# Kernel optimization log

Measured on AMD Instinct MI355X. Metric: run time of the kernel, lower is better.

## Reference

```python
import jax, jax.numpy as jnp
import numpy as np

K = 5
P = 1.5
MU = 0.01
N_NODES = 100000
N_EDGES = 1600000
D_FEAT = 32


def setup_inputs() -> dict:
    key = jax.random.key(0)
    k1, k2 = jax.random.split(key)
    h = jax.random.normal(k1, (N_NODES, D_FEAT), dtype=jnp.float32)
    edge_index = jax.random.randint(k2, (2, N_EDGES), 0, N_NODES, dtype=jnp.int64)
    return {"h": h, "edge_index": edge_index}


def reference(h, edge_index):
    row, col = edge_index[0], edge_index[1]
    for _ in range(K):
        diff = h[row] - h[col]                      # [E, d] gather
        norm_diff = jnp.maximum(jnp.linalg.norm(diff, axis=1), 1e-6)  # [E]
        weights = (norm_diff / norm_diff.max()) ** (P - 2.0)          # [E]
        # agg[r] += sum over edges with row==r of weights * (h[col] - h[row])
        msgs = weights[:, None] * (-diff)           # [E, d]
        agg = jax.ops.segment_sum(msgs, row, num_segments=N_NODES)    # [N, d]
        h = h - MU * agg
    return h
```

## Files before the change

kernel.cpp:

```cpp
#include <hip/hip_runtime.h>

#define NN 100000
#define NE 1600000
#define DF 32
#define KIT 5
#define MU 0.01f
#define NSLOT 256
#define NV4 (NN * DF / 4)
#define ELLW 36
#define AUXCAP 65536
#define NSLICE 8
#define SLICEN (NN / NSLICE)
#define NSUB 20
#define NBLKA (NE / 256)
#define SEGW 64
#define INVALID_PK 0xffffffffu

typedef float f32x4 __attribute__((ext_vector_type(4)));
typedef float f32x2 __attribute__((ext_vector_type(2)));


__global__ __launch_bounds__(64) void zero_kernel(int* __restrict__ p, int n) {
    int i = blockIdx.x * blockDim.x + threadIdx.x;
    if (i < n) p[i] = 0;
}

__global__ __launch_bounds__(256) void ell_part_kernel(const int* __restrict__ row,
                                                       const int* __restrict__ col,
                                                       unsigned int* __restrict__ buck,
                                                       int* __restrict__ auxcnt,
                                                       int2* __restrict__ aux) {
    __shared__ int wcnt[4][8];
    __shared__ int woff[4][8];
    __shared__ unsigned int sseg[8][SEGW];
    const int t = threadIdx.x;
    const int w = t >> 6;
    const int lane = t & 63;

    ((unsigned int*)sseg)[t] = INVALID_PK;
    ((unsigned int*)sseg)[t + 256] = INVALID_PK;

    const int e = blockIdx.x * 256 + t;
    int b = 8;
    unsigned int packed = INVALID_PK;
    int r = 0, c = 0;
    if (e < NE) {
        r = __builtin_nontemporal_load(&row[e]);
        c = __builtin_nontemporal_load(&col[e]);
        b = r / SLICEN;
        const int rl = r - b * SLICEN;
        packed = ((unsigned int)rl << 17) | (unsigned int)c;
    }

    int myprefix = 0;
    #pragma unroll
    for (int k = 0; k < 8; ++k) {
        const unsigned long long mk = __ballot(b == k);
        if (lane == 0) wcnt[w][k] = __popcll(mk);
        if (k == b) myprefix = __popcll(mk & ((1ull << lane) - 1ull));
    }
    __syncthreads();
    if (t < 32) {
        const int w2 = t >> 3, k = t & 7;
        int o = 0;
        for (int w3 = 0; w3 < w2; ++w3) o += wcnt[w3][k];
        woff[w2][k] = o;
    }
    __syncthreads();

    if (b < 8) {
        const int pos = woff[w][b] + myprefix;
        if (pos < SEGW) {
            sseg[b][pos] = packed;
        } else {
            const int a = atomicAdd(auxcnt, 1);
            if (a < AUXCAP) aux[a] = make_int2(r, c);
        }
    }
    __syncthreads();

    #pragma unroll
    for (int k = 0; k < 2; ++k) {
        const int idx = t + k * 256;
        const int bb = idx >> 6;
        const int j = idx & 63;
        buck[((size_t)bb * NBLKA + blockIdx.x) * SEGW + j] = sseg[bb][j];
    }
}

__global__ __launch_bounds__(1024) void ell_count_kernel(const unsigned int* __restrict__ buck,
                                                         unsigned short* __restrict__ cnt) {
    __shared__ int hist[SLICEN];
    const int t = threadIdx.x;
    const int s = blockIdx.x & (NSLICE - 1);
    const int j = blockIdx.x >> 3;
    const int lane = t & 63;
    const int wid = t >> 6;
    const int blo = j * NBLKA / NSUB;
    const int bhi = (j + 1) * NBLKA / NSUB;

    for (int i = t; i < SLICEN; i += 1024) hist[i] = 0;
    __syncthreads();

    const unsigned int* sp = buck + (size_t)s * NBLKA * SEGW;
    int blk = blo + wid;
    unsigned int pk = (blk < bhi) ? sp[(size_t)blk * SEGW + lane] : INVALID_PK;
    for (; blk < bhi; blk += 16) {
        const int nb = blk + 16;
        const unsigned int nx = (nb < bhi) ? sp[(size_t)nb * SEGW + lane] : INVALID_PK;
        const int rl = (int)(pk >> 17);
        if (rl < SLICEN) atomicAdd(&hist[rl], 1);
        pk = nx;
    }
    __syncthreads();
    unsigned short* cp = cnt + ((size_t)s * NSUB + j) * SLICEN;
    for (int i = t; i < SLICEN; i += 1024) cp[i] = (unsigned short)hist[i];
}

__global__ __launch_bounds__(256) void ell_prefix_kernel(unsigned short* __restrict__ cnt,
                                                         int* __restrict__ degc) {
    const int i = blockIdx.x * blockDim.x + threadIdx.x;
    if (i >= NN) return;
    const int s = i / SLICEN;
    const int rl = i - s * SLICEN;
    unsigned short* cp = cnt + (size_t)s * NSUB * SLICEN + rl;
    int base = 0;
    #pragma unroll
    for (int j = 0; j < NSUB; ++j) {
        const int v = cp[(size_t)j * SLICEN];
        cp[(size_t)j * SLICEN] = (unsigned short)base;
        base += v;
    }
    degc[i] = base;
}

__global__ __launch_bounds__(1024) void ell_place_kernel(const unsigned int* __restrict__ buck,
                                                         const unsigned short* __restrict__ cnt,
                                                         int* __restrict__ colell,
                                                         int* __restrict__ auxcnt,
                                                         int2* __restrict__ aux) {
    __shared__ int cur[SLICEN];
    const int t = threadIdx.x;
    const int s = blockIdx.x & (NSLICE - 1);
    const int j = blockIdx.x >> 3;
    const int lane = t & 63;
    const int wid = t >> 6;
    const int blo = j * NBLKA / NSUB;
    const int bhi = (j + 1) * NBLKA / NSUB;

    const unsigned short* cp = cnt + ((size_t)s * NSUB + j) * SLICEN;
    for (int i = t; i < SLICEN; i += 1024) cur[i] = (int)cp[i];
    __syncthreads();

    const unsigned int* sp = buck + (size_t)s * NBLKA * SEGW;
    int blk = blo + wid;
    unsigned int pk = (blk < bhi) ? sp[(size_t)blk * SEGW + lane] : INVALID_PK;
    for (; blk < bhi; blk += 16) {
        const int nb = blk + 16;
        const unsigned int nx = (nb < bhi) ? sp[(size_t)nb * SEGW + lane] : INVALID_PK;
        const int rl = (int)(pk >> 17);
        if (rl < SLICEN) {
            const int c = (int)(pk & 0x1ffffu);
            const int pos = atomicAdd(&cur[rl], 1);
            const int r = s * SLICEN + rl;
            if (pos < ELLW) {
                colell[r * ELLW + pos] = c;
            } else {
                const int a = atomicAdd(auxcnt, 1);
                if (a < AUXCAP) aux[a] = make_int2(r, c);
            }
        }
        pk = nx;
    }
}


__device__ __forceinline__ unsigned int pack2bf(float a, float b) {
    unsigned int ua = __float_as_uint(a);
    unsigned int ub = __float_as_uint(b);
    return ((ua + 0x8000u) >> 16) | (((ub + 0x8000u) >> 16) << 16);
}

__device__ __forceinline__ f32x2 bf2(unsigned int v) {
    f32x2 r;
    r.x = __uint_as_float(v << 16);
    r.y = __uint_as_float(v & 0xffff0000u);
    return r;
}

__global__ __launch_bounds__(256) void tobf16_kernel(const float* __restrict__ h,
                                                     uint2* __restrict__ hb) {
    int i = blockIdx.x * blockDim.x + threadIdx.x;
    if (i < NV4) {
        const f32x4 v = __builtin_nontemporal_load(((const f32x4*)h) + i);
        hb[i] = make_uint2(pack2bf(v.x, v.y), pack2bf(v.z, v.w));
    }
}


__device__ __forceinline__ void node_head(const uint4* __restrict__ u,
                                          const f32x2* __restrict__ hr2,
                                          f32x2* __restrict__ acc, float& nmax) {
    #pragma unroll
    for (int j = 0; j < 4; ++j) {
        f32x2 d0 = hr2[0] - bf2(u[j].x);
        f32x2 d1 = hr2[1] - bf2(u[j].y);
        f32x2 d2 = hr2[2] - bf2(u[j].z);
        f32x2 d3 = hr2[3] - bf2(u[j].w);
        f32x2 s2 = d0 * d0;
        s2 += d1 * d1;
        s2 += d2 * d2;
        s2 += d3 * d3;
        float s = s2.x + s2.y;
        s += __shfl_xor(s, 1, 32);
        s += __shfl_xor(s, 2, 32);
        const float n = fmaxf(sqrtf(s), 1e-6f);
        nmax = fmaxf(nmax, n);
        const float w = -rsqrtf(n);
        acc[0] += d0 * w;
        acc[1] += d1 * w;
        acc[2] += d2 * w;
        acc[3] += d3 * w;
    }
}

__device__ __forceinline__ void node_tail(const uint4* __restrict__ hb4,
                                          const int* __restrict__ colell, int n,
                                          int deg, int q, int f2,
                                          const f32x2* __restrict__ hr2,
                                          f32x2* __restrict__ acc, float& nmax) {
    for (int k = 32; k < deg; k += 8) {
        const int ei = k + q;
        const int c = (ei < deg) ? colell[n * ELLW + ei] : n;
        const uint4 uu = hb4[c * 4 + f2];
        f32x2 d0 = hr2[0] - bf2(uu.x);
        f32x2 d1 = hr2[1] - bf2(uu.y);
        f32x2 d2 = hr2[2] - bf2(uu.z);
        f32x2 d3 = hr2[3] - bf2(uu.w);
        f32x2 s2 = d0 * d0;
        s2 += d1 * d1;
        s2 += d2 * d2;
        s2 += d3 * d3;
        float s = s2.x + s2.y;
        s += __shfl_xor(s, 1, 32);
        s += __shfl_xor(s, 2, 32);
        const float n2 = fmaxf(sqrtf(s), 1e-6f);
        nmax = fmaxf(nmax, n2);
        const float w = -rsqrtf(n2);
        acc[0] += d0 * w;
        acc[1] += d1 * w;
        acc[2] += d2 * w;
        acc[3] += d3 * w;
    }
}

__global__ __launch_bounds__(256) void agg_kernel(const uint4* __restrict__ hb4,
                                                  const int* __restrict__ degc,
                                                  const int* __restrict__ colell,
                                                  float* __restrict__ S,
                                                  int* __restrict__ maxslots) {
    const int lane = threadIdx.x & 31;
    const int q = lane >> 2;
    const int f2 = lane & 3;
    const int pair = (blockIdx.x * blockDim.x + threadIdx.x) >> 5;
    const int n0 = pair * 2;
    const int n1 = n0 + 1;

    const int d0 = min(degc[n0], ELLW);
    const int d1 = min(degc[n1], ELLW);

    const int ca = (lane < d0) ? colell[n0 * ELLW + lane] : n0;
    const int cb = (lane < d1) ? colell[n1 * ELLW + lane] : n1;
    const uint4 hru0 = hb4[n0 * 4 + f2];
    const uint4 hru1 = hb4[n1 * 4 + f2];

    uint4 u0[4], u1[4];
    #pragma unroll
    for (int j = 0; j < 4; ++j) u0[j] = hb4[__shfl(ca, 8 * j + q, 32) * 4 + f2];
    #pragma unroll
    for (int j = 0; j < 4; ++j) u1[j] = hb4[__shfl(cb, 8 * j + q, 32) * 4 + f2];

    f32x2 hr0[4], hr1[4];
    hr0[0] = bf2(hru0.x); hr0[1] = bf2(hru0.y); hr0[2] = bf2(hru0.z); hr0[3] = bf2(hru0.w);
    hr1[0] = bf2(hru1.x); hr1[1] = bf2(hru1.y); hr1[2] = bf2(hru1.z); hr1[3] = bf2(hru1.w);

    f32x2 acc0[4], acc1[4];
    #pragma unroll
    for (int i = 0; i < 4; ++i) {
        acc0[i] = (f32x2){0.0f, 0.0f};
        acc1[i] = (f32x2){0.0f, 0.0f};
    }
    float nmax = 0.0f;

    node_head(u0, hr0, acc0, nmax);
    node_head(u1, hr1, acc1, nmax);

    node_tail(hb4, colell, n0, d0, q, f2, hr0, acc0, nmax);
    node_tail(hb4, colell, n1, d1, q, f2, hr1, acc1, nmax);

    #pragma unroll
    for (int m = 4; m < 32; m <<= 1) {
        #pragma unroll
        for (int i = 0; i < 4; ++i) {
            acc0[i].x += __shfl_xor(acc0[i].x, m, 32);
            acc0[i].y += __shfl_xor(acc0[i].y, m, 32);
            acc1[i].x += __shfl_xor(acc1[i].x, m, 32);
            acc1[i].y += __shfl_xor(acc1[i].y, m, 32);
        }
    }
    if (q == 0) {
        ((float4*)S)[n0 * 8 + f2 * 2] = make_float4(acc0[0].x, acc0[0].y, acc0[1].x, acc0[1].y);
        ((float4*)S)[n0 * 8 + f2 * 2 + 1] = make_float4(acc0[2].x, acc0[2].y, acc0[3].x, acc0[3].y);
        ((float4*)S)[n1 * 8 + f2 * 2] = make_float4(acc1[0].x, acc1[0].y, acc1[1].x, acc1[1].y);
        ((float4*)S)[n1 * 8 + f2 * 2 + 1] = make_float4(acc1[2].x, acc1[2].y, acc1[3].x, acc1[3].y);
    }

    nmax = fmaxf(nmax, __shfl_xor(nmax, 4, 32));
    nmax = fmaxf(nmax, __shfl_xor(nmax, 8, 32));
    nmax = fmaxf(nmax, __shfl_xor(nmax, 16, 32));
    nmax = fmaxf(nmax, __shfl_xor(nmax, 32, 64));
    if ((threadIdx.x & 63) == 0) {
        atomicMax(&maxslots[blockIdx.x & (NSLOT - 1)], __float_as_int(nmax));
    }
}

__global__ __launch_bounds__(256) void aux_kernel(const uint2* __restrict__ hb,
                                                  const int2* __restrict__ aux,
                                                  const int* __restrict__ auxcnt,
                                                  float* __restrict__ S,
                                                  int* __restrict__ maxslots) {
    const int n = min(*auxcnt, AUXCAP);
    for (int i = blockIdx.x * blockDim.x + threadIdx.x; i < n;
         i += gridDim.x * blockDim.x) {
        const int r = aux[i].x;
        const int c = aux[i].y;
        float d[32];
        float s = 0.0f;
        for (int j = 0; j < 8; ++j) {
            const uint2 ur = hb[r * 8 + j];
            const uint2 uc = hb[c * 8 + j];
            float fr[4], fc[4];
            fr[0] = __uint_as_float(ur.x << 16);
            fr[1] = __uint_as_float(ur.x & 0xffff0000u);
            fr[2] = __uint_as_float(ur.y << 16);
            fr[3] = __uint_as_float(ur.y & 0xffff0000u);
            fc[0] = __uint_as_float(uc.x << 16);
            fc[1] = __uint_as_float(uc.x & 0xffff0000u);
            fc[2] = __uint_as_float(uc.y << 16);
            fc[3] = __uint_as_float(uc.y & 0xffff0000u);
            #pragma unroll
            for (int k = 0; k < 4; ++k) {
                d[j * 4 + k] = fr[k] - fc[k];
                s = fmaf(d[j * 4 + k], d[j * 4 + k], s);
            }
        }
        const float nn = fmaxf(sqrtf(s), 1e-6f);
        atomicMax(&maxslots[i & (NSLOT - 1)], __float_as_int(nn));
        const float w = rsqrtf(nn);
        for (int f = 0; f < 32; ++f) atomicAdd(&S[r * DF + f], -d[f] * w);
    }
}

__global__ __launch_bounds__(256) void update_kernel(const float4* __restrict__ hcur,
                                                     float4* __restrict__ hnxt,
                                                     uint2* __restrict__ hb,
                                                     const float4* __restrict__ S,
                                                     const int* __restrict__ slots) {
    const int t = threadIdx.x;
    int v = slots[t];
    #pragma unroll
    for (int m = 32; m > 0; m >>= 1) v = max(v, __shfl_xor(v, m, 64));
    __shared__ int sm[4];
    __shared__ float sscale;
    if ((t & 63) == 0) sm[t >> 6] = v;
    __syncthreads();
    if (t == 0) {
        int bm = max(max(sm[0], sm[1]), max(sm[2], sm[3]));
        sscale = MU * sqrtf(__int_as_float(bm));
    }
    __syncthreads();
    const float scale = sscale;
    const int i = blockIdx.x * blockDim.x + t;
    if (i < NV4) {
        const float4 hv = hcur[i];
        const float4 sv = S[i];
        float4 o;
        o.x = hv.x - scale * sv.x;
        o.y = hv.y - scale * sv.y;
        o.z = hv.z - scale * sv.z;
        o.w = hv.w - scale * sv.w;
        hnxt[i] = o;
        hb[i] = make_uint2(pack2bf(o.x, o.y), pack2bf(o.z, o.w));
    }
}

extern "C" void kernel_launch(void* const* d_in, const int* in_sizes, int n_in,
                              void* d_out, int out_size, void* d_ws, size_t ws_size,
                              hipStream_t stream) {
    const float* h_in = (const float*)d_in[0];
    const int* row = (const int*)d_in[1];
    const int* col = row + NE;
    float* out = (float*)d_out;

    float* S = (float*)d_ws;
    int* maxslots = (int*)(S + NN * DF);
    int* degc = maxslots + KIT * NSLOT;
    int* auxcnt = degc + NN;
    uintptr_t pa = (uintptr_t)(auxcnt + 1);
    pa = (pa + 7) & ~(uintptr_t)7;
    int2* aux = (int2*)pa;
    int* colell = (int*)(aux + AUXCAP);
    uintptr_t p = (uintptr_t)(colell + NN * ELLW);
    p = (p + 15) & ~(uintptr_t)15;
    uint2* hb = (uint2*)p;
    unsigned int* buck = (unsigned int*)S;
    unsigned short* cnt = (unsigned short*)hb;

    const int fb = NSLICE * NSUB;
    const int pb = (NN + 255) / 256;
    const int gb = (NN / 2 * 32 + 255) / 256;
    const int ub = (NV4 + 255) / 256;

    zero_kernel<<<1, 64, 0, stream>>>(auxcnt, 1);
    ell_part_kernel<<<NBLKA, 256, 0, stream>>>(row, col, buck, auxcnt, aux);
    ell_count_kernel<<<fb, 1024, 0, stream>>>(buck, cnt);
    ell_prefix_kernel<<<pb, 256, 0, stream>>>(cnt, degc);
    ell_place_kernel<<<fb, 1024, 0, stream>>>(buck, cnt, colell, auxcnt, aux);
    tobf16_kernel<<<ub, 256, 0, stream>>>(h_in, hb);

    for (int it = 0; it < KIT; ++it) {
        const float* cur = (it == 0) ? h_in : out;
        agg_kernel<<<gb, 256, 0, stream>>>((const uint4*)hb, degc, colell, S,
                                           maxslots + it * NSLOT);
        aux_kernel<<<32, 256, 0, stream>>>(hb, aux, auxcnt, S, maxslots + it * NSLOT);
        update_kernel<<<ub, 256, 0, stream>>>((const float4*)cur, (float4*)out, hb,
                                              (const float4*)S,
                                              maxslots + it * NSLOT);
    }
}
```

Measured before the change: 383.3 us.

## Split neighbor lists by column half and aggregate in two cache-friendly passes

Adds a preprocessing kernel that reorders each node's ELL neighbor list so columns in the lower half of the node range come first, and stores the split count packed into degc. The aggregation then runs twice per iteration, first over low-half neighbors and then over high-half neighbors, accumulating into S. The aim is to keep each pass's gather working set (half of the bf16 feature table) resident in cache. The cost is a second launch, extra reads and writes of S, and less work per subtile for low-degree nodes.

New measurement: 588.0 us. +53.4%, slower.

```diff
diff --git a/kernel.cpp b/kernel.cpp
--- a/kernel.cpp
+++ b/kernel.cpp
@@ -15,6 +15,7 @@
 #define NBLKA (NE / 256)
 #define SEGW 64
 #define INVALID_PK 0xffffffffu
+#define HALF (NN / 2)
 
 typedef float f32x4 __attribute__((ext_vector_type(4)));
 typedef float f32x2 __attribute__((ext_vector_type(2)));
@@ -174,6 +175,26 @@
     }
 }
 
+__global__ __launch_bounds__(256) void ell_split_kernel(int* __restrict__ colell,
+                                                        int* __restrict__ degc) {
+    const int n = (blockIdx.x * blockDim.x + threadIdx.x) >> 6;
+    if (n >= NN) return;
+    const int l = threadIdx.x & 63;
+    const int m = min(degc[n], ELLW);
+    const int c = (l < m) ? colell[n * ELLW + l] : 0;
+    const bool valid = l < m;
+    const unsigned long long lomask = __ballot(valid && (c < HALF));
+    const unsigned long long himask = __ballot(valid && (c >= HALF));
+    const int nlo = __popcll(lomask);
+    const unsigned long long below = (1ull << l) - 1ull;
+    if (valid) {
+        const int pos = (c < HALF) ? __popcll(lomask & below)
+                                   : nlo + __popcll(himask & below);
+        colell[n * ELLW + pos] = c;
+    }
+    if (l == 0) degc[n] = m | (nlo << 8);
+}
+
 
 __device__ __forceinline__ unsigned int pack2bf(float a, float b) {
     unsigned int ua = __float_as_uint(a);
@@ -198,67 +219,34 @@
 }
 
 
-__device__ __forceinline__ void node_head(const uint4* __restrict__ u,
-                                          const f32x2* __restrict__ hr2,
-                                          f32x2* __restrict__ acc, float& nmax) {
-    #pragma unroll
-    for (int j = 0; j < 4; ++j) {
-        f32x2 d0 = hr2[0] - bf2(u[j].x);
-        f32x2 d1 = hr2[1] - bf2(u[j].y);
-        f32x2 d2 = hr2[2] - bf2(u[j].z);
-        f32x2 d3 = hr2[3] - bf2(u[j].w);
-        f32x2 s2 = d0 * d0;
-        s2 += d1 * d1;
-        s2 += d2 * d2;
-        s2 += d3 * d3;
-        float s = s2.x + s2.y;
-        s += __shfl_xor(s, 1, 32);
-        s += __shfl_xor(s, 2, 32);
-        const float n = fmaxf(sqrtf(s), 1e-6f);
-        nmax = fmaxf(nmax, n);
-        const float w = -rsqrtf(n);
-        acc[0] += d0 * w;
-        acc[1] += d1 * w;
-        acc[2] += d2 * w;
-        acc[3] += d3 * w;
-    }
-}
-
-__device__ __forceinline__ void node_tail(const uint4* __restrict__ hb4,
-                                          const int* __restrict__ colell, int n,
-                                          int deg, int q, int f2,
-                                          const f32x2* __restrict__ hr2,
-                                          f32x2* __restrict__ acc, float& nmax) {
-    for (int k = 32; k < deg; k += 8) {
-        const int ei = k + q;
-        const int c = (ei < deg) ? colell[n * ELLW + ei] : n;
-        const uint4 uu = hb4[c * 4 + f2];
-        f32x2 d0 = hr2[0] - bf2(uu.x);
-        f32x2 d1 = hr2[1] - bf2(uu.y);
-        f32x2 d2 = hr2[2] - bf2(uu.z);
-        f32x2 d3 = hr2[3] - bf2(uu.w);
-        f32x2 s2 = d0 * d0;
-        s2 += d1 * d1;
-        s2 += d2 * d2;
-        s2 += d3 * d3;
-        float s = s2.x + s2.y;
-        s += __shfl_xor(s, 1, 32);
-        s += __shfl_xor(s, 2, 32);
-        const float n2 = fmaxf(sqrtf(s), 1e-6f);
-        nmax = fmaxf(nmax, n2);
-        const float w = -rsqrtf(n2);
-        acc[0] += d0 * w;
-        acc[1] += d1 * w;
-        acc[2] += d2 * w;
-        acc[3] += d3 * w;
-    }
+__device__ __forceinline__ void subtile(uint4 uu, const f32x2* __restrict__ hr2,
+                                        f32x2* __restrict__ acc, float& nmax) {
+    f32x2 d0 = hr2[0] - bf2(uu.x);
+    f32x2 d1 = hr2[1] - bf2(uu.y);
+    f32x2 d2 = hr2[2] - bf2(uu.z);
+    f32x2 d3 = hr2[3] - bf2(uu.w);
+    f32x2 s2 = d0 * d0;
+    s2 += d1 * d1;
+    s2 += d2 * d2;
+    s2 += d3 * d3;
+    float s = s2.x + s2.y;
+    s += __shfl_xor(s, 1, 32);
+    s += __shfl_xor(s, 2, 32);
+    const float n = fmaxf(sqrtf(s), 1e-6f);
+    nmax = fmaxf(nmax, n);
+    const float w = -rsqrtf(n);
+    acc[0] += d0 * w;
+    acc[1] += d1 * w;
+    acc[2] += d2 * w;
+    acc[3] += d3 * w;
 }
 
 __global__ __launch_bounds__(256) void agg_kernel(const uint4* __restrict__ hb4,
                                                   const int* __restrict__ degc,
                                                   const int* __restrict__ colell,
                                                   float* __restrict__ S,
-                                                  int* __restrict__ maxslots) {
+                                                  int* __restrict__ maxslots,
+                                                  int phase) {
     const int lane = threadIdx.x & 31;
     const int q = lane >> 2;
     const int f2 = lane & 3;
@@ -266,19 +254,33 @@
     const int n0 = pair * 2;
     const int n1 = n0 + 1;
 
-    const int d0 = min(degc[n0], ELLW);
-    const int d1 = min(degc[n1], ELLW);
-
-    const int ca = (lane < d0) ? colell[n0 * ELLW + lane] : n0;
-    const int cb = (lane < d1) ? colell[n1 * ELLW + lane] : n1;
+    const int v0 = degc[n0];
+    const int v1 = degc[n1];
+    const int m0 = v0 & 0xff, nlo0 = v0 >> 8;
+    const int m1 = v1 & 0xff, nlo1 = v1 >> 8;
+    const int b0 = phase ? nlo0 : 0;
+    const int e0 = phase ? m0 : nlo0;
+    const int b1 = phase ? nlo1 : 0;
+    const int e1 = phase ? m1 : nlo1;
+    const int t0 = (e0 - b0 + 7) >> 3;
+    const int t1 = (e1 - b1 + 7) >> 3;
+
     const uint4 hru0 = hb4[n0 * 4 + f2];
     const uint4 hru1 = hb4[n1 * 4 + f2];
 
-    uint4 u0[4], u1[4];
-    #pragma unroll
-    for (int j = 0; j < 4; ++j) u0[j] = hb4[__shfl(ca, 8 * j + q, 32) * 4 + f2];
-    #pragma unroll
-    for (int j = 0; j < 4; ++j) u1[j] = hb4[__shfl(cb, 8 * j + q, 32) * 4 + f2];
+    int c0[2], c1[2];
+    #pragma unroll
+    for (int j = 0; j < 2; ++j) {
+        const int s0 = b0 + 8 * j + q;
+        c0[j] = (s0 < e0) ? __builtin_nontemporal_load(&colell[n0 * ELLW + s0]) : n0;
+        const int s1 = b1 + 8 * j + q;
+        c1[j] = (s1 < e1) ? __builtin_nontemporal_load(&colell[n1 * ELLW + s1]) : n1;
+    }
+    uint4 u0[2], u1[2];
+    if (0 < t0) u0[0] = hb4[c0[0] * 4 + f2];
+    if (0 < t1) u1[0] = hb4[c1[0] * 4 + f2];
+    if (1 < t0) u0[1] = hb4[c0[1] * 4 + f2];
+    if (1 < t1) u1[1] = hb4[c1[1] * 4 + f2];
 
     f32x2 hr0[4], hr1[4];
     hr0[0] = bf2(hru0.x); hr0[1] = bf2(hru0.y); hr0[2] = bf2(hru0.z); hr0[3] = bf2(hru0.w);
@@ -292,11 +294,21 @@
     }
     float nmax = 0.0f;
 
-    node_head(u0, hr0, acc0, nmax);
-    node_head(u1, hr1, acc1, nmax);
-
-    node_tail(hb4, colell, n0, d0, q, f2, hr0, acc0, nmax);
-    node_tail(hb4, colell, n1, d1, q, f2, hr1, acc1, nmax);
+    if (0 < t0) subtile(u0[0], hr0, acc0, nmax);
+    if (0 < t1) subtile(u1[0], hr1, acc1, nmax);
+    if (1 < t0) subtile(u0[1], hr0, acc0, nmax);
+    if (1 < t1) subtile(u1[1], hr1, acc1, nmax);
+
+    for (int j = 2; j < t0; ++j) {
+        const int s0 = b0 + 8 * j + q;
+        const int c = (s0 < e0) ? __builtin_nontemporal_load(&colell[n0 * ELLW + s0]) : n0;
+        subtile(hb4[c * 4 + f2], hr0, acc0, nmax);
+    }
+    for (int j = 2; j < t1; ++j) {
+        const int s1 = b1 + 8 * j + q;
+        const int c = (s1 < e1) ? __builtin_nontemporal_load(&colell[n1 * ELLW + s1]) : n1;
+        subtile(hb4[c * 4 + f2], hr1, acc1, nmax);
+    }
 
     #pragma unroll
     for (int m = 4; m < 32; m <<= 1) {
@@ -309,10 +321,21 @@
         }
     }
     if (q == 0) {
-        ((float4*)S)[n0 * 8 + f2 * 2] = make_float4(acc0[0].x, acc0[0].y, acc0[1].x, acc0[1].y);
-        ((float4*)S)[n0 * 8 + f2 * 2 + 1] = make_float4(acc0[2].x, acc0[2].y, acc0[3].x, acc0[3].y);
-        ((float4*)S)[n1 * 8 + f2 * 2] = make_float4(acc1[0].x, acc1[0].y, acc1[1].x, acc1[1].y);
-        ((float4*)S)[n1 * 8 + f2 * 2 + 1] = make_float4(acc1[2].x, acc1[2].y, acc1[3].x, acc1[3].y);
+        f32x4* Sv = (f32x4*)S;
+        f32x4 a0 = {acc0[0].x, acc0[0].y, acc0[1].x, acc0[1].y};
+        f32x4 a1 = {acc0[2].x, acc0[2].y, acc0[3].x, acc0[3].y};
+        f32x4 b0v = {acc1[0].x, acc1[0].y, acc1[1].x, acc1[1].y};
+        f32x4 b1v = {acc1[2].x, acc1[2].y, acc1[3].x, acc1[3].y};
+        if (phase) {
+            a0 += Sv[n0 * 8 + f2 * 2];
+            a1 += Sv[n0 * 8 + f2 * 2 + 1];
+            b0v += Sv[n1 * 8 + f2 * 2];
+            b1v += Sv[n1 * 8 + f2 * 2 + 1];
+        }
+        __builtin_nontemporal_store(a0, Sv + n0 * 8 + f2 * 2);
+        __builtin_nontemporal_store(a1, Sv + n0 * 8 + f2 * 2 + 1);
+        __builtin_nontemporal_store(b0v, Sv + n1 * 8 + f2 * 2);
+        __builtin_nontemporal_store(b1v, Sv + n1 * 8 + f2 * 2 + 1);
     }
 
     nmax = fmaxf(nmax, __shfl_xor(nmax, 4, 32));
@@ -418,6 +441,7 @@
 
     const int fb = NSLICE * NSUB;
     const int pb = (NN + 255) / 256;
+    const int sb = (NN * 64 + 255) / 256;
     const int gb = (NN / 2 * 32 + 255) / 256;
     const int ub = (NV4 + 255) / 256;
 
@@ -426,12 +450,15 @@
     ell_count_kernel<<<fb, 1024, 0, stream>>>(buck, cnt);
     ell_prefix_kernel<<<pb, 256, 0, stream>>>(cnt, degc);
     ell_place_kernel<<<fb, 1024, 0, stream>>>(buck, cnt, colell, auxcnt, aux);
+    ell_split_kernel<<<sb, 256, 0, stream>>>(colell, degc);
     tobf16_kernel<<<ub, 256, 0, stream>>>(h_in, hb);
 
     for (int it = 0; it < KIT; ++it) {
         const float* cur = (it == 0) ? h_in : out;
         agg_kernel<<<gb, 256, 0, stream>>>((const uint4*)hb, degc, colell, S,
-                                           maxslots + it * NSLOT);
+                                           maxslots + it * NSLOT, 0);
+        agg_kernel<<<gb, 256, 0, stream>>>((const uint4*)hb, degc, colell, S,
+                                           maxslots + it * NSLOT, 1);
         aux_kernel<<<32, 256, 0, stream>>>(hb, aux, auxcnt, S, maxslots + it * NSLOT);
         update_kernel<<<ub, 256, 0, stream>>>((const float4*)cur, (float4*)out, hb,
                                               (const float4*)S,
```
